# Kernel tuning notes

Hardware: AMD Instinct MI355X
Metric: run time of the kernel (lower is better)

## Reference

```python
import jax, jax.numpy as jnp
import numpy as np
from jax import lax


def setup_inputs() -> dict:
    key = jax.random.key(0)
    kx, kw = jax.random.split(key)
    x = jax.random.normal(kx, (8, 32, 16, 160, 160), dtype=jnp.float32)
    # xavier-normal-ish init (scale irrelevant to correctness testing)
    weights = jax.random.normal(kw, (32, 32, 1, 3, 3), dtype=jnp.float32) * 0.1
    return {"x": x, "weights": weights}


def reference(x, weights):
    # per-(out_ch, in_ch) scale: mean |w| over kernel dims (2,3,4), detached
    scale = lax.stop_gradient(jnp.mean(jnp.abs(weights), axis=(2, 3, 4), keepdims=True))
    binary_no_grad = scale * jnp.sign(weights)          # {+-scale}
    clipped = jnp.clip(weights, -1.0, 1.0)
    # straight-through estimator: value = binary_no_grad, grad flows via clipped
    binary_weights = lax.stop_gradient(binary_no_grad - clipped) + clipped
    out = lax.conv_general_dilated(
        x, binary_weights,
        window_strides=(1, 1, 1),
        padding=((0, 0), (1, 1), (1, 1)),
        rhs_dilation=(1, 1, 1),
        dimension_numbers=("NCDHW", "OIDHW", "NCDHW"),
        feature_group_count=1,
    )
    return out
```

## Files before the change

### kernel.cpp

```cpp
#include <hip/hip_runtime.h>


typedef _Float16 half8 __attribute__((ext_vector_type(8)));
typedef float    floatx4 __attribute__((ext_vector_type(4)));

#define DHW  409600
#define HW   25600

__global__ __launch_bounds__(512, 4) void bnn_conv3d_kernel(
        const float* __restrict__ x, const float* __restrict__ w,
        float* __restrict__ out) {
    __shared__ __align__(16) _Float16 ldsh[31104];

    const int tid  = threadIdx.x;
    const int lane = tid & 63;
    const int wid  = tid >> 6;

    const int bid = blockIdx.x;
    const int ht  = bid % 40;
    const int nd  = bid / 40;
    const int d   = nd & 15;
    const int n   = nd >> 4;
    const int h0  = ht * 4;

    #pragma unroll
    for (int p4 = 0; p4 < 2; ++p4) {
        const int oi = tid * 2 + p4;
        const int o  = oi >> 5;
        const int i  = oi & 31;
        const float* wp = w + oi * 9;
        float s = 0.f;
        #pragma unroll
        for (int t = 0; t < 9; ++t) s += fabsf(wp[t]);
        s *= (1.f / 9.f);
        const int l = ((i >> 3) << 4) | (o & 15);
        const int p = o >> 4;
        const int j = i & 7;
        #pragma unroll
        for (int t = 0; t < 9; ++t) {
            const float v  = wp[t];
            const float sg = (v > 0.f) ? 1.f : ((v < 0.f) ? -1.f : 0.f);
            ldsh[((t * 2 + p) * 64 + l) * 8 + j] = (_Float16)(s * sg);
        }
    }
    __syncthreads();

    half8 wf[2][9];
    {
        const half8* fb = reinterpret_cast<const half8*>(ldsh);
        #pragma unroll
        for (int t = 0; t < 9; ++t) {
            wf[0][t] = fb[(t * 2 + 0) * 64 + lane];
            wf[1][t] = fb[(t * 2 + 1) * 64 + lane];
        }
    }
    __syncthreads();


    if (tid < 192) {
        const int pos = tid >> 4, word = tid & 15;
        const int r   = pos >> 1;
        const int w1  = (pos & 1) ? 161 : 0;
        reinterpret_cast<unsigned int*>(ldsh)[(r * 162 + w1) * 16 + word] = 0u;
    }
    #pragma unroll 2
    for (int it = 0; it < 8; ++it) {
        const int idx = it * 512 + tid;
        if (idx < 3840) {
            const int wpos = idx % 160;
            const int rest = idx / 160;
            const int kg   = rest & 3;
            const int r    = rest >> 2;
            const int h_in = h0 - 1 + r;
            float v[8];
            if ((unsigned)h_in < 160u) {
                const float* src = x + ((n * 32 + kg * 8) * 16 + d) * HW
                                     + h_in * 160 + wpos;
                #pragma unroll
                for (int c = 0; c < 8; ++c) v[c] = src[c * DHW];
            } else {
                #pragma unroll
                for (int c = 0; c < 8; ++c) v[c] = 0.f;
            }
            half8 pk;
            #pragma unroll
            for (int c = 0; c < 8; ++c) pk[c] = (_Float16)v[c];
            const int w1  = wpos + 1;
            const int skg = kg ^ ((w1 >> 1) & 3);
            *reinterpret_cast<half8*>(&ldsh[(r * 162 + w1) * 32 + skg * 8]) = pk;
        }
    }
    __syncthreads();

    const int s16   = lane & 15;
    const int kg    = lane >> 4;
    const int row   = wid & 3;
    const int whalf = wid >> 2;
    const int h     = h0 + row;
    const int obase = (n * 32 + s16) * DHW + d * HW + h * 160 + kg * 4;

    #pragma unroll
    for (int wtl = 0; wtl < 5; ++wtl) {
        const int wbase = (whalf * 5 + wtl) * 16;
        floatx4 acc0 = {0.f, 0.f, 0.f, 0.f};
        floatx4 acc1 = {0.f, 0.f, 0.f, 0.f};
        #pragma unroll
        for (int kh = 0; kh < 3; ++kh) {
            const int rrow = (row + kh) * 162;
            #pragma unroll
            for (int kw = 0; kw < 3; ++kw) {
                const int w1   = wbase + s16 + kw;
                const int aidx = (rrow + w1) * 32 + ((kg ^ ((w1 >> 1) & 3)) * 8);
                const half8 a  = *reinterpret_cast<const half8*>(&ldsh[aidx]);
                const int t = kh * 3 + kw;
                acc0 = __builtin_amdgcn_mfma_f32_16x16x32_f16(a, wf[0][t], acc0, 0, 0, 0);
                acc1 = __builtin_amdgcn_mfma_f32_16x16x32_f16(a, wf[1][t], acc1, 0, 0, 0);
            }
        }
        float* op = out + obase + wbase;
        *reinterpret_cast<floatx4*>(op)            = acc0;
        *reinterpret_cast<floatx4*>(op + 16 * DHW) = acc1;
    }
}

extern "C" void kernel_launch(void* const* d_in, const int* in_sizes, int n_in,
                              void* d_out, int out_size, void* d_ws, size_t ws_size,
                              hipStream_t stream) {
    const float* x = (const float*)d_in[0];
    const float* w = (const float*)d_in[1];
    float* out = (float*)d_out;
    bnn_conv3d_kernel<<<dim3(5120), dim3(512), 0, stream>>>(x, w, out);
}
```

Baseline: 223.9 us.

## Precompute binarized weights in a prep kernel and batch x loads before LDS stores

Moves per-block weight binarization into a one-block prep kernel that writes fp16 MFMA fragments to workspace, which the conv kernel then loads directly from global memory. This removes redundant per-block weight processing and two barriers. It also issues all input loads into registers before converting and storing them to LDS, to increase outstanding memory requests. The cost is an extra kernel launch and much higher register pressure under the occupancy bound, which could cause spills.

```diff
diff --git a/kernel.cpp b/kernel.cpp
--- a/kernel.cpp
+++ b/kernel.cpp
@@ -7,8 +7,33 @@
 #define DHW  409600
 #define HW   25600
 
+__global__ void bnn_wprep_kernel(const float* __restrict__ w,
+                                 _Float16* __restrict__ ws) {
+    const int tid = threadIdx.x;
+    #pragma unroll
+    for (int p4 = 0; p4 < 4; ++p4) {
+        const int oi = tid * 4 + p4;
+        const int o  = oi >> 5;
+        const int i  = oi & 31;
+        const float* wp = w + oi * 9;
+        float s = 0.f;
+        #pragma unroll
+        for (int t = 0; t < 9; ++t) s += fabsf(wp[t]);
+        s *= (1.f / 9.f);
+        const int l = ((i >> 3) << 4) | (o & 15);
+        const int p = o >> 4;
+        const int j = i & 7;
+        #pragma unroll
+        for (int t = 0; t < 9; ++t) {
+            const float v  = wp[t];
+            const float sg = (v > 0.f) ? 1.f : ((v < 0.f) ? -1.f : 0.f);
+            ws[((t * 2 + p) * 64 + l) * 8 + j] = (_Float16)(s * sg);
+        }
+    }
+}
+
 __global__ __launch_bounds__(512, 4) void bnn_conv3d_kernel(
-        const float* __restrict__ x, const float* __restrict__ w,
+        const float* __restrict__ x, const _Float16* __restrict__ ws,
         float* __restrict__ out) {
     __shared__ __align__(16) _Float16 ldsh[31104];
 
@@ -23,39 +48,26 @@
     const int n   = nd >> 4;
     const int h0  = ht * 4;
 
+    float xv[8][8];
     #pragma unroll
-    for (int p4 = 0; p4 < 2; ++p4) {
-        const int oi = tid * 2 + p4;
-        const int o  = oi >> 5;
-        const int i  = oi & 31;
-        const float* wp = w + oi * 9;
-        float s = 0.f;
-        #pragma unroll
-        for (int t = 0; t < 9; ++t) s += fabsf(wp[t]);
-        s *= (1.f / 9.f);
-        const int l = ((i >> 3) << 4) | (o & 15);
-        const int p = o >> 4;
-        const int j = i & 7;
-        #pragma unroll
-        for (int t = 0; t < 9; ++t) {
-            const float v  = wp[t];
-            const float sg = (v > 0.f) ? 1.f : ((v < 0.f) ? -1.f : 0.f);
-            ldsh[((t * 2 + p) * 64 + l) * 8 + j] = (_Float16)(s * sg);
+    for (int it = 0; it < 8; ++it) {
+        const bool active = (it < 7) || (tid < 256);
+        const int idx  = it * 512 + tid;
+        const int wpos = idx % 160;
+        const int rest = idx / 160;
+        const int kg   = rest & 3;
+        const int r    = rest >> 2;
+        const int h_in = h0 - 1 + r;
+        if (active && (unsigned)h_in < 160u) {
+            const float* src = x + ((n * 32 + kg * 8) * 16 + d) * HW
+                                 + h_in * 160 + wpos;
+            #pragma unroll
+            for (int c = 0; c < 8; ++c) xv[it][c] = src[c * DHW];
+        } else {
+            #pragma unroll
+            for (int c = 0; c < 8; ++c) xv[it][c] = 0.f;
         }
     }
-    __syncthreads();
-
-    half8 wf[2][9];
-    {
-        const half8* fb = reinterpret_cast<const half8*>(ldsh);
-        #pragma unroll
-        for (int t = 0; t < 9; ++t) {
-            wf[0][t] = fb[(t * 2 + 0) * 64 + lane];
-            wf[1][t] = fb[(t * 2 + 1) * 64 + lane];
-        }
-    }
-    __syncthreads();
-
 
     if (tid < 192) {
         const int pos = tid >> 4, word = tid & 15;
@@ -63,34 +75,35 @@
         const int w1  = (pos & 1) ? 161 : 0;
         reinterpret_cast<unsigned int*>(ldsh)[(r * 162 + w1) * 16 + word] = 0u;
     }
-    #pragma unroll 2
+
+    #pragma unroll
     for (int it = 0; it < 8; ++it) {
-        const int idx = it * 512 + tid;
-        if (idx < 3840) {
+        const bool active = (it < 7) || (tid < 256);
+        if (active) {
+            const int idx  = it * 512 + tid;
             const int wpos = idx % 160;
             const int rest = idx / 160;
             const int kg   = rest & 3;
             const int r    = rest >> 2;
-            const int h_in = h0 - 1 + r;
-            float v[8];
-            if ((unsigned)h_in < 160u) {
-                const float* src = x + ((n * 32 + kg * 8) * 16 + d) * HW
-                                     + h_in * 160 + wpos;
-                #pragma unroll
-                for (int c = 0; c < 8; ++c) v[c] = src[c * DHW];
-            } else {
-                #pragma unroll
-                for (int c = 0; c < 8; ++c) v[c] = 0.f;
-            }
             half8 pk;
             #pragma unroll
-            for (int c = 0; c < 8; ++c) pk[c] = (_Float16)v[c];
+            for (int c = 0; c < 8; ++c) pk[c] = (_Float16)xv[it][c];
             const int w1  = wpos + 1;
             const int skg = kg ^ ((w1 >> 1) & 3);
             *reinterpret_cast<half8*>(&ldsh[(r * 162 + w1) * 32 + skg * 8]) = pk;
         }
     }
     __syncthreads();
+
+    half8 wf[2][9];
+    {
+        const half8* fb = reinterpret_cast<const half8*>(ws);
+        #pragma unroll
+        for (int t = 0; t < 9; ++t) {
+            wf[0][t] = fb[(t * 2 + 0) * 64 + lane];
+            wf[1][t] = fb[(t * 2 + 1) * 64 + lane];
+        }
+    }
 
     const int s16   = lane & 15;
     const int kg    = lane >> 4;
@@ -129,5 +142,7 @@
     const float* x = (const float*)d_in[0];
     const float* w = (const float*)d_in[1];
     float* out = (float*)d_out;
-    bnn_conv3d_kernel<<<dim3(5120), dim3(512), 0, stream>>>(x, w, out);
+    _Float16* ws = (_Float16*)d_ws;
+    bnn_wprep_kernel<<<dim3(1), dim3(256), 0, stream>>>(w, ws);
+    bnn_conv3d_kernel<<<dim3(5120), dim3(512), 0, stream>>>(x, ws, out);
 }
```

Result: slower. 229.0 us (+2.2%).
